# Kernel tuning notes

Hardware: AMD Instinct MI355X
Metric: run time of the kernel (lower is better)

Reference implementation:

```python
import jax, jax.numpy as jnp
import numpy as np

N_USER = 1_000_000
N_ITEM = 100_000
E = 16          # embedding_size
O = 16          # out_size per head
H = 4           # head_num
HID = 32        # hidden_size
B = 8192        # batch
S = 200         # sample_num
L = 50          # history length
NSUPP = 50_000  # supp_user_num


def _xavier(key, shape):
    fan_in, fan_out = shape[-2], shape[-1]
    std = np.sqrt(2.0 / (fan_in + fan_out))
    return (jax.random.normal(key, shape) * std).astype(jnp.float32)


def setup_inputs() -> dict:
    key = jax.random.key(0)
    ks = jax.random.split(key, 16)
    uid = jax.random.randint(ks[0], (B,), 0, N_USER)
    iid = jax.random.randint(ks[1], (B,), 0, N_ITEM)
    return {
        "user_embedding": _xavier(ks[2], (N_USER, E)),
        "item_embedding": _xavier(ks[3], (N_ITEM, E)),
        "wq": _xavier(ks[4], (H, E, O)),   # per-head Wq (no bias)
        "wk": _xavier(ks[5], (H, E, O)),
        "wv": _xavier(ks[6], (H, O, O)),
        "w_out": _xavier(ks[7], (H * O, O)),
        "l1_w": _xavier(ks[8], (3 * E, HID)),
        "l1_b": jnp.full((HID,), 0.1, jnp.float32),
        "l2_w": _xavier(ks[9], (HID, HID // 2)),
        "l2_b": jnp.full((HID // 2,), 0.1, jnp.float32),
        "l3_w": _xavier(ks[10], (HID // 2, 1)),
        "l3_b": jnp.full((1,), 0.1, jnp.float32),
        "user_bias": jnp.zeros((N_USER, 1), jnp.float32),
        "item_bias": jnp.zeros((N_ITEM, 1), jnp.float32),
        "x": jnp.stack([uid, iid], axis=1),                          # [B,2]
        "history": jax.random.randint(ks[11], (B, L), 0, N_ITEM),    # [B,L]
        "history_len": jax.random.randint(ks[12], (B,), 1, L + 1),   # [B] >=1
        "supp_users": jax.random.randint(ks[13], (NSUPP,), 0, N_USER),
        "sample_index": jax.random.randint(ks[14], (H, B, S), 0, NSUPP),
    }


def reference(user_embedding, item_embedding, wq, wk, wv, w_out,
              l1_w, l1_b, l2_w, l2_b, l3_w, l3_b, user_bias, item_bias,
              x, history, history_len, supp_users, sample_index):
    user_id = x[:, 0]
    item_id = x[:, 1]

    # user init embedding = mean-by-len of full (unmasked) history, as in source
    hist_emb = item_embedding[history]                                # [B,L,E]
    user_init = hist_emb.sum(axis=1) / history_len[:, None].astype(jnp.float32)  # [B,E]

    # per-head GAT over sampled support users (all heads vectorized)
    nb = user_embedding[supp_users[sample_index]]                     # [H,B,S,E]
    q = jnp.einsum('be,heo->hbo', user_init, wq)                      # [H,B,O]
    k = jnp.einsum('hbse,heo->hbso', nb, wk)                          # [H,B,S,O]
    attn = jax.nn.softmax(jnp.einsum('hbo,hbso->hbs', q, k), axis=-1)
    ctx = jnp.einsum('hbs,hbso->hbo', attn, k)                        # [H,B,O]
    gat = jnp.einsum('hbo,hop->hbp', ctx, wv)                         # [H,B,O]
    gat = jnp.transpose(gat, (1, 0, 2)).reshape(B, H * O)             # concat heads

    user_emb = gat @ w_out                                            # [B,O]
    item_emb = item_embedding[item_id]                                # [B,E]
    interaction = user_emb * item_emb
    ratings = interaction.sum(axis=1)

    h = jnp.concatenate([user_emb, item_emb, interaction], axis=1)    # [B,3E]
    x1 = jnp.tanh(h @ l1_w + l1_b)
    x2 = jnp.tanh(x1 @ l2_w + l2_b)
    x3 = (x2 @ l3_w + l3_b).reshape(-1)

    ub = user_bias[user_id, 0]
    ib = item_bias[item_id, 0]
    return (ratings + x3) / 2.0 + ub + ib
```

## Files before the change

kernel.cpp:

```cpp
#include <hip/hip_runtime.h>
#include <math.h>

#define N_USERS 1000000
#define N_ITEMS 100000
#define EMB 16
#define OUTD 16
#define NH 4
#define HID 32
#define BB 8192
#define SS 200
#define LL 50
#define NSUPP 50000

typedef float v4f __attribute__((ext_vector_type(4)));
typedef _Float16 h4 __attribute__((ext_vector_type(4)));
typedef _Float16 h2 __attribute__((ext_vector_type(2)));

__global__ __launch_bounds__(256) void prep_kernel(
    const float* __restrict__ user_emb,
    const int*   __restrict__ supp_users,
    const float* __restrict__ wk,
    _Float16*    __restrict__ Ksupp,
    const float* __restrict__ item_emb,
    const int*   __restrict__ history,
    const int*   __restrict__ history_len,
    const float* __restrict__ wq,
    float*       __restrict__ qbuf)
{
    __shared__ float s_wk[NH * EMB * OUTD];
    __shared__ float s_u[16][EMB];
    __shared__ float s_ui[4][EMB];
    __shared__ float s_wq[NH * EMB * OUTD];

    int t = threadIdx.x;
    if (blockIdx.x < NSUPP / 16) {
        for (int i = t; i < NH * EMB * OUTD; i += 256) s_wk[i] = wk[i];
        int n0 = blockIdx.x * 16;
        {
            int ul = t >> 4, e = t & 15;
            int row = supp_users[n0 + ul];
            s_u[ul][e] = user_emb[(size_t)row * EMB + e];
        }
        __syncthreads();
        int h   = t >> 6;
        int sub = (t >> 4) & 3;
        int o   = t & 15;
#pragma unroll
        for (int r = 0; r < 4; ++r) {
            int ul = sub + 4 * r;
            float acc = 0.f;
#pragma unroll
            for (int e = 0; e < EMB; ++e)
                acc += s_u[ul][e] * s_wk[(h * EMB + e) * OUTD + o];
            Ksupp[((size_t)h * NSUPP + n0 + ul) * OUTD + o] = (_Float16)acc;
        }
    } else {
        for (int i = t; i < NH * EMB * OUTD; i += 256) s_wq[i] = wq[i];
        int g    = t >> 6;
        int lane = t & 63;
        int l4   = lane >> 4;
        int e    = lane & 15;
        int b    = (blockIdx.x - NSUPP / 16) * 4 + g;

        float sum = 0.f;
        for (int l = l4; l < LL; l += 4) {
            int it = __builtin_nontemporal_load(history + (size_t)b * LL + l);
            sum += item_emb[(size_t)it * EMB + e];
        }
        sum += __shfl_xor(sum, 16);
        sum += __shfl_xor(sum, 32);
        if (lane < EMB) s_ui[g][lane] = sum / (float)history_len[b];
        __syncthreads();

        int h = (t >> 4) & 3;
        int o = t & 15;
        float acc = 0.f;
#pragma unroll
        for (int ee = 0; ee < EMB; ++ee)
            acc += s_ui[g][ee] * s_wq[(h * EMB + ee) * OUTD + o];
        qbuf[((size_t)b * NH + h) * OUTD + o] = acc;
    }
}

__global__ __launch_bounds__(256, 8) void attn_kernel(
    const _Float16* __restrict__ Ksupp,
    const float* __restrict__ qbuf,
    const int*   __restrict__ sample_index,
    const float* __restrict__ wv,
    float*       __restrict__ gat)
{
    int blk   = blockIdx.x;
    int h     = (blk & 7) >> 1;
    int btile = ((blk >> 3) << 1) | (blk & 1);
    int wave  = threadIdx.x >> 6;
    int lane  = threadIdx.x & 63;
    int b     = btile * 4 + wave;
    int g     = lane >> 2;
    int qt    = lane & 3;

    const int* si = sample_index + ((size_t)h * BB + b) * SS;
    int pre0 = __builtin_nontemporal_load(si + lane);
    int pre1 = __builtin_nontemporal_load(si + lane + 64);
    int pre2 = __builtin_nontemporal_load(si + lane + 128);
    int pre3 = (lane < 8) ? __builtin_nontemporal_load(si + lane + 192) : 0;

    v4f qv = __builtin_nontemporal_load(
        (const v4f*)(qbuf + ((size_t)b * NH + h) * OUTD) + qt);
    h4 qh = __builtin_convertvector(qv, h4);
    h2 qlo = {qh.x, qh.y};
    h2 qhi = {qh.z, qh.w};

    const h4* K4 = (const h4*)(Ksupp + (size_t)h * NSUPP * OUTD);

    int idx[13];
#pragma unroll
    for (int r = 0; r < 13; ++r) {
        int pre = (r < 4) ? pre0 : (r < 8) ? pre1 : (r < 12) ? pre2 : pre3;
        idx[r] = __shfl(pre, (r & 3) * 16 + g, 64);
    }

    h4 kq[13];
#pragma unroll
    for (int r = 0; r < 13; ++r)
        kq[r] = K4[idx[r] * 4 + qt];

    float l = 0.f;
    v4f c = {0.f, 0.f, 0.f, 0.f};
#pragma unroll
    for (int r = 0; r < 13; ++r) {
        h2 klo = {kq[r].x, kq[r].y};
        h2 khi = {kq[r].z, kq[r].w};
        float p = __builtin_amdgcn_fdot2(klo, qlo,
                  __builtin_amdgcn_fdot2(khi, qhi, 0.f, false), false);
        p += __shfl_xor(p, 1);
        p += __shfl_xor(p, 2);
        float w = __expf(p);
        if (r == 12) w = (g < 8) ? w : 0.f;
        l += w;
        v4f kf = __builtin_convertvector(kq[r], v4f);
        c += w * kf;
    }
#pragma unroll
    for (int off = 4; off < 64; off <<= 1) {
        l   += __shfl_xor(l, off);
        c.x += __shfl_xor(c.x, off);
        c.y += __shfl_xor(c.y, off);
        c.z += __shfl_xor(c.z, off);
        c.w += __shfl_xor(c.w, off);
    }
    float inv = 1.f / l;

    float part = c.x * wv[((size_t)h * OUTD + qt * 4 + 0) * OUTD + g]
               + c.y * wv[((size_t)h * OUTD + qt * 4 + 1) * OUTD + g]
               + c.z * wv[((size_t)h * OUTD + qt * 4 + 2) * OUTD + g]
               + c.w * wv[((size_t)h * OUTD + qt * 4 + 3) * OUTD + g];
    part += __shfl_xor(part, 1);
    part += __shfl_xor(part, 2);
    if (qt == 0)
        gat[(size_t)b * (NH * OUTD) + h * OUTD + g] = part * inv;
}

__global__ __launch_bounds__(256) void epilogue_kernel(
    const float* __restrict__ gat,
    const float* __restrict__ item_emb,
    const float* __restrict__ w_out,
    const float* __restrict__ l1_w, const float* __restrict__ l1_b,
    const float* __restrict__ l2_w, const float* __restrict__ l2_b,
    const float* __restrict__ l3_w, const float* __restrict__ l3_b,
    const float* __restrict__ user_bias, const float* __restrict__ item_bias,
    const int*   __restrict__ x,
    float*       __restrict__ out)
{
    int t    = threadIdx.x;
    int g    = t >> 6;
    int lane = t & 63;
    int b    = blockIdx.x * 4 + g;

    __shared__ float s_gat[4][NH * OUTD];
    __shared__ float s_ue[4][OUTD];
    __shared__ float s_ie[4][EMB];
    __shared__ float s_x1[4][HID];
    __shared__ float s_x2[4][HID / 2];

    int uid = x[(size_t)b * 2 + 0];
    int iid = x[(size_t)b * 2 + 1];

    s_gat[g][lane] = gat[(size_t)b * (NH * OUTD) + lane];
    if (lane < EMB) s_ie[g][lane] = item_emb[(size_t)iid * EMB + lane];
    __syncthreads();

    if (lane < OUTD) {
        float acc = 0.f;
#pragma unroll
        for (int j = 0; j < NH * OUTD; ++j) acc += s_gat[g][j] * w_out[j * OUTD + lane];
        s_ue[g][lane] = acc;
    }
    __syncthreads();

    if (lane < HID) {
        float acc = l1_b[lane];
#pragma unroll
        for (int i = 0; i < EMB; ++i) {
            float ue = s_ue[g][i], ie = s_ie[g][i];
            acc += ue * l1_w[i * HID + lane]
                 + ie * l1_w[(EMB + i) * HID + lane]
                 + ue * ie * l1_w[(2 * EMB + i) * HID + lane];
        }
        s_x1[g][lane] = tanhf(acc);
    }
    __syncthreads();

    if (lane < HID / 2) {
        float acc = l2_b[lane];
#pragma unroll
        for (int j = 0; j < HID; ++j) acc += s_x1[g][j] * l2_w[j * (HID / 2) + lane];
        s_x2[g][lane] = tanhf(acc);
    }
    __syncthreads();

    if (lane == 0) {
        float x3 = l3_b[0];
#pragma unroll
        for (int j = 0; j < HID / 2; ++j) x3 += s_x2[g][j] * l3_w[j];
        float ratings = 0.f;
#pragma unroll
        for (int o = 0; o < OUTD; ++o) ratings += s_ue[g][o] * s_ie[g][o];
        out[b] = 0.5f * (ratings + x3) + user_bias[uid] + item_bias[iid];
    }
}

extern "C" void kernel_launch(void* const* d_in, const int* in_sizes, int n_in,
                              void* d_out, int out_size, void* d_ws, size_t ws_size,
                              hipStream_t stream) {
    const float* user_embedding = (const float*)d_in[0];
    const float* item_embedding = (const float*)d_in[1];
    const float* wq             = (const float*)d_in[2];
    const float* wk             = (const float*)d_in[3];
    const float* wv             = (const float*)d_in[4];
    const float* w_out          = (const float*)d_in[5];
    const float* l1_w           = (const float*)d_in[6];
    const float* l1_b           = (const float*)d_in[7];
    const float* l2_w           = (const float*)d_in[8];
    const float* l2_b           = (const float*)d_in[9];
    const float* l3_w           = (const float*)d_in[10];
    const float* l3_b           = (const float*)d_in[11];
    const float* user_bias      = (const float*)d_in[12];
    const float* item_bias      = (const float*)d_in[13];
    const int*   x              = (const int*)d_in[14];
    const int*   history        = (const int*)d_in[15];
    const int*   history_len    = (const int*)d_in[16];
    const int*   supp_users     = (const int*)d_in[17];
    const int*   sample_index   = (const int*)d_in[18];
    float* out = (float*)d_out;

    char* ws = (char*)d_ws;
    _Float16* Ksupp = (_Float16*)ws;
    ws += (size_t)NH * NSUPP * OUTD * sizeof(_Float16);
    float* qbuf  = (float*)ws;
    ws += (size_t)BB * NH * OUTD * sizeof(float);
    float* gat   = (float*)ws;

    prep_kernel<<<NSUPP / 16 + BB / 4, 256, 0, stream>>>(
        user_embedding, supp_users, wk, Ksupp,
        item_embedding, history, history_len, wq, qbuf);
    attn_kernel<<<NH * BB / 4, 256, 0, stream>>>(Ksupp, qbuf, sample_index, wv, gat);
    epilogue_kernel<<<BB / 4, 256, 0, stream>>>(
        gat, item_embedding, w_out, l1_w, l1_b, l2_w, l2_b, l3_w, l3_b,
        user_bias, item_bias, x, out);
}
```

Measured before the change: 220.1 us.

## Use 16-byte K row loads with two lanes per sample in attention

The attention kernel now assigns two lanes per sampled neighbour, each loading 8 fp16 values (16 bytes), instead of four lanes each loading 4 values. This halves the gather instructions and the intra-group dot-product shuffles, and the last partial round is skipped for inactive lanes. In exchange the final reduction over 8 accumulators needs more cross-lane shuffles, register use rises, and the occupancy hint in launch bounds is lowered from 8 to 4.

```diff
diff --git a/kernel.cpp b/kernel.cpp
--- a/kernel.cpp
+++ b/kernel.cpp
@@ -13,8 +13,10 @@
 #define NSUPP 50000
 
 typedef float v4f __attribute__((ext_vector_type(4)));
+typedef float v8f __attribute__((ext_vector_type(8)));
+typedef _Float16 h2 __attribute__((ext_vector_type(2)));
 typedef _Float16 h4 __attribute__((ext_vector_type(4)));
-typedef _Float16 h2 __attribute__((ext_vector_type(2)));
+typedef _Float16 h8 __attribute__((ext_vector_type(8)));
 
 __global__ __launch_bounds__(256) void prep_kernel(
     const float* __restrict__ user_emb,
@@ -82,7 +84,7 @@
     }
 }
 
-__global__ __launch_bounds__(256, 8) void attn_kernel(
+__global__ __launch_bounds__(256, 4) void attn_kernel(
     const _Float16* __restrict__ Ksupp,
     const float* __restrict__ qbuf,
     const int*   __restrict__ sample_index,
@@ -95,8 +97,8 @@
     int wave  = threadIdx.x >> 6;
     int lane  = threadIdx.x & 63;
     int b     = btile * 4 + wave;
-    int g     = lane >> 2;
-    int qt    = lane & 3;
+    int g2    = lane >> 1;
+    int pr    = lane & 1;
 
     const int* si = sample_index + ((size_t)h * BB + b) * SS;
     int pre0 = __builtin_nontemporal_load(si + lane);
@@ -104,60 +106,68 @@
     int pre2 = __builtin_nontemporal_load(si + lane + 128);
     int pre3 = (lane < 8) ? __builtin_nontemporal_load(si + lane + 192) : 0;
 
-    v4f qv = __builtin_nontemporal_load(
-        (const v4f*)(qbuf + ((size_t)b * NH + h) * OUTD) + qt);
-    h4 qh = __builtin_convertvector(qv, h4);
-    h2 qlo = {qh.x, qh.y};
-    h2 qhi = {qh.z, qh.w};
-
-    const h4* K4 = (const h4*)(Ksupp + (size_t)h * NSUPP * OUTD);
-
-    int idx[13];
-#pragma unroll
-    for (int r = 0; r < 13; ++r) {
-        int pre = (r < 4) ? pre0 : (r < 8) ? pre1 : (r < 12) ? pre2 : pre3;
-        idx[r] = __shfl(pre, (r & 3) * 16 + g, 64);
-    }
-
-    h4 kq[13];
-#pragma unroll
-    for (int r = 0; r < 13; ++r)
-        kq[r] = K4[idx[r] * 4 + qt];
+    const v4f* qrow = (const v4f*)(qbuf + ((size_t)b * NH + h) * OUTD);
+    v4f qa = __builtin_nontemporal_load(qrow + pr * 2);
+    v4f qb = __builtin_nontemporal_load(qrow + pr * 2 + 1);
+    h4 qha = __builtin_convertvector(qa, h4);
+    h4 qhb = __builtin_convertvector(qb, h4);
+    h2 q0 = {qha.x, qha.y}, q1 = {qha.z, qha.w};
+    h2 q2 = {qhb.x, qhb.y}, q3 = {qhb.z, qhb.w};
+
+    const h8* K8 = (const h8*)(Ksupp + (size_t)h * NSUPP * OUTD);
+
+    int idx[7];
+#pragma unroll
+    for (int r = 0; r < 7; ++r) {
+        int pre = (r < 2) ? pre0 : (r < 4) ? pre1 : (r < 6) ? pre2 : pre3;
+        idx[r] = __shfl(pre, (r & 1) * 32 + g2, 64);
+    }
+
+    h8 kq[7];
+#pragma unroll
+    for (int r = 0; r < 6; ++r)
+        kq[r] = K8[(size_t)idx[r] * 2 + pr];
+    {
+        h8 kz = {};
+        if (g2 < 8) kz = K8[(size_t)idx[6] * 2 + pr];
+        kq[6] = kz;
+    }
 
     float l = 0.f;
-    v4f c = {0.f, 0.f, 0.f, 0.f};
-#pragma unroll
-    for (int r = 0; r < 13; ++r) {
-        h2 klo = {kq[r].x, kq[r].y};
-        h2 khi = {kq[r].z, kq[r].w};
-        float p = __builtin_amdgcn_fdot2(klo, qlo,
-                  __builtin_amdgcn_fdot2(khi, qhi, 0.f, false), false);
+    v8f c = {0.f, 0.f, 0.f, 0.f, 0.f, 0.f, 0.f, 0.f};
+#pragma unroll
+    for (int r = 0; r < 7; ++r) {
+        h2 k0 = __builtin_shufflevector(kq[r], kq[r], 0, 1);
+        h2 k1 = __builtin_shufflevector(kq[r], kq[r], 2, 3);
+        h2 k2 = __builtin_shufflevector(kq[r], kq[r], 4, 5);
+        h2 k3 = __builtin_shufflevector(kq[r], kq[r], 6, 7);
+        float p = __builtin_amdgcn_fdot2(k0, q0,
+                  __builtin_amdgcn_fdot2(k1, q1,
+                  __builtin_amdgcn_fdot2(k2, q2,
+                  __builtin_amdgcn_fdot2(k3, q3, 0.f, false), false), false), false);
         p += __shfl_xor(p, 1);
-        p += __shfl_xor(p, 2);
         float w = __expf(p);
-        if (r == 12) w = (g < 8) ? w : 0.f;
+        if (r == 6) w = (g2 < 8) ? w : 0.f;
         l += w;
-        v4f kf = __builtin_convertvector(kq[r], v4f);
-        c += w * kf;
-    }
-#pragma unroll
-    for (int off = 4; off < 64; off <<= 1) {
-        l   += __shfl_xor(l, off);
-        c.x += __shfl_xor(c.x, off);
-        c.y += __shfl_xor(c.y, off);
-        c.z += __shfl_xor(c.z, off);
-        c.w += __shfl_xor(c.w, off);
+        c += w * __builtin_convertvector(kq[r], v8f);
+    }
+
+#pragma unroll
+    for (int off = 2; off < 64; off <<= 1) {
+        l += __shfl_xor(l, off);
+#pragma unroll
+        for (int j = 0; j < 8; ++j) c[j] += __shfl_xor(c[j], off);
     }
     float inv = 1.f / l;
 
-    float part = c.x * wv[((size_t)h * OUTD + qt * 4 + 0) * OUTD + g]
-               + c.y * wv[((size_t)h * OUTD + qt * 4 + 1) * OUTD + g]
-               + c.z * wv[((size_t)h * OUTD + qt * 4 + 2) * OUTD + g]
-               + c.w * wv[((size_t)h * OUTD + qt * 4 + 3) * OUTD + g];
+    int pcol = g2 & 15;
+    const float* wvh = wv + ((size_t)h * OUTD + pr * 8) * OUTD + pcol;
+    float part = 0.f;
+#pragma unroll
+    for (int j = 0; j < 8; ++j) part += c[j] * wvh[(size_t)j * OUTD];
     part += __shfl_xor(part, 1);
-    part += __shfl_xor(part, 2);
-    if (qt == 0)
-        gat[(size_t)b * (NH * OUTD) + h * OUTD + g] = part * inv;
+    if (pr == 0 && g2 < 16)
+        gat[(size_t)b * (NH * OUTD) + h * OUTD + pcol] = part * inv;
 }
 
 __global__ __launch_bounds__(256) void epilogue_kernel(
```

Result: no change. 219.2 us (-0.4%).

## Stream support-key tiles through LDS and walk sorted sample indices per block

Applied to the files above, without the earlier changes.

The attention kernel now gives each block 128 batch rows of one head. Each wave bitonic-sorts its rows' 200 sample indices and stores them in shared memory. The block then streams the whole per-head K table through double-buffered LDS tiles of 1024 rows, and each row consumes its sorted indices that fall inside the current tile. This swaps random global gathers for sequential streaming plus LDS lookups, which is meant to cut scattered memory traffic. The cost is that every block reads all 50k keys per head, pays for the in-register sort, and runs a divergent ballot-driven inner loop, with larger LDS use and low occupancy.

```diff
diff --git a/kernel.cpp b/kernel.cpp
--- a/kernel.cpp
+++ b/kernel.cpp
@@ -12,9 +12,15 @@
 #define LL 50
 #define NSUPP 50000
 
+#define TT 1024
+#define NT ((NSUPP + TT - 1) / TT)
+#define GB 128
+
 typedef float v4f __attribute__((ext_vector_type(4)));
+typedef float v8f __attribute__((ext_vector_type(8)));
+typedef _Float16 h2 __attribute__((ext_vector_type(2)));
 typedef _Float16 h4 __attribute__((ext_vector_type(4)));
-typedef _Float16 h2 __attribute__((ext_vector_type(2)));
+typedef _Float16 h8 __attribute__((ext_vector_type(8)));
 
 __global__ __launch_bounds__(256) void prep_kernel(
     const float* __restrict__ user_emb,
@@ -82,82 +88,178 @@
     }
 }
 
-__global__ __launch_bounds__(256, 8) void attn_kernel(
+__global__ __launch_bounds__(512, 2) void attn_kernel(
     const _Float16* __restrict__ Ksupp,
     const float* __restrict__ qbuf,
     const int*   __restrict__ sample_index,
     const float* __restrict__ wv,
     float*       __restrict__ gat)
 {
+    __shared__ __align__(16) _Float16 s_tile[2][TT * OUTD];
+    __shared__ unsigned short s_idx[GB * 256];
+
     int blk   = blockIdx.x;
     int h     = (blk & 7) >> 1;
     int btile = ((blk >> 3) << 1) | (blk & 1);
     int wave  = threadIdx.x >> 6;
     int lane  = threadIdx.x & 63;
-    int b     = btile * 4 + wave;
+    int tid   = threadIdx.x;
     int g     = lane >> 2;
     int qt    = lane & 3;
 
-    const int* si = sample_index + ((size_t)h * BB + b) * SS;
-    int pre0 = __builtin_nontemporal_load(si + lane);
-    int pre1 = __builtin_nontemporal_load(si + lane + 64);
-    int pre2 = __builtin_nontemporal_load(si + lane + 128);
-    int pre3 = (lane < 8) ? __builtin_nontemporal_load(si + lane + 192) : 0;
-
-    v4f qv = __builtin_nontemporal_load(
-        (const v4f*)(qbuf + ((size_t)b * NH + h) * OUTD) + qt);
-    h4 qh = __builtin_convertvector(qv, h4);
-    h2 qlo = {qh.x, qh.y};
-    h2 qhi = {qh.z, qh.w};
-
-    const h4* K4 = (const h4*)(Ksupp + (size_t)h * NSUPP * OUTD);
-
-    int idx[13];
-#pragma unroll
-    for (int r = 0; r < 13; ++r) {
-        int pre = (r < 4) ? pre0 : (r < 8) ? pre1 : (r < 12) ? pre2 : pre3;
-        idx[r] = __shfl(pre, (r & 3) * 16 + g, 64);
-    }
-
-    h4 kq[13];
-#pragma unroll
-    for (int r = 0; r < 13; ++r)
-        kq[r] = K4[idx[r] * 4 + qt];
+    const char* Khb = (const char*)(Ksupp + (size_t)h * NSUPP * OUTD);
+    int b_base = btile * GB;
+
+    v4f st[4];
+#pragma unroll
+    for (int m = 0; m < 4; ++m)
+        st[m] = *(const v4f*)(Khb + (size_t)(m * 512 + tid) * 16);
+
+    {
+        const int* si0 = sample_index + ((size_t)h * BB + (b_base + wave * 16)) * SS;
+        unsigned n0 = (unsigned)__builtin_nontemporal_load(si0 + lane);
+        unsigned n1 = (unsigned)__builtin_nontemporal_load(si0 + 64 + lane);
+        unsigned n2 = (unsigned)__builtin_nontemporal_load(si0 + 128 + lane);
+        unsigned n3 = (lane < SS - 192) ?
+            (unsigned)__builtin_nontemporal_load(si0 + 192 + lane) : 0xFFFFu;
+        for (int bs = 0; bs < 16; ++bs) {
+            unsigned v[4] = {n0, n1, n2, n3};
+            if (bs < 15) {
+                const int* si = si0 + (size_t)(bs + 1) * SS;
+                n0 = (unsigned)__builtin_nontemporal_load(si + lane);
+                n1 = (unsigned)__builtin_nontemporal_load(si + 64 + lane);
+                n2 = (unsigned)__builtin_nontemporal_load(si + 128 + lane);
+                n3 = (lane < SS - 192) ?
+                    (unsigned)__builtin_nontemporal_load(si + 192 + lane) : 0xFFFFu;
+            }
+#pragma unroll
+            for (int kk = 2; kk <= 256; kk <<= 1) {
+#pragma unroll
+                for (int j = kk >> 1; j > 0; j >>= 1) {
+                    if (j >= 64) {
+                        const int jr = j >> 6;
+#pragma unroll
+                        for (int r = 0; r < 4; ++r) {
+                            if ((r & jr) == 0) {
+                                const int rp = r | jr;
+                                bool up = (((unsigned)(r * 64) & (unsigned)kk) == 0u);
+                                unsigned a = v[r], bq = v[rp];
+                                unsigned mn = a < bq ? a : bq;
+                                unsigned mx = a < bq ? bq : a;
+                                v[r]  = up ? mn : mx;
+                                v[rp] = up ? mx : mn;
+                            }
+                        }
+                    } else {
+#pragma unroll
+                        for (int r = 0; r < 4; ++r) {
+                            unsigned a = v[r];
+                            unsigned p = (unsigned)__shfl_xor((int)a, j, 64);
+                            int e = r * 64 + lane;
+                            bool lower = ((e & j) == 0);
+                            bool up    = ((e & kk) == 0);
+                            unsigned mn = a < p ? a : p;
+                            unsigned mx = a < p ? p : a;
+                            v[r] = (up == lower) ? mn : mx;
+                        }
+                    }
+                }
+            }
+            int bl = wave * 16 + bs;
+            s_idx[bl * 256 +       lane] = (unsigned short)v[0];
+            s_idx[bl * 256 +  64 + lane] = (unsigned short)v[1];
+            s_idx[bl * 256 + 128 + lane] = (unsigned short)v[2];
+            s_idx[bl * 256 + 192 + lane] = (unsigned short)v[3];
+        }
+    }
+
+    int b_local = wave * 16 + g;
+    int bfull   = b_base + b_local;
+    const v4f* qrow = (const v4f*)(qbuf + ((size_t)bfull * NH + h) * OUTD);
+    h4 A = __builtin_convertvector(qrow[0], h4);
+    h4 Bv = __builtin_convertvector(qrow[1], h4);
+    h4 Cv = __builtin_convertvector(qrow[2], h4);
+    h4 Dv = __builtin_convertvector(qrow[3], h4);
+    h2 q0 = {A.x, A.y},  q1 = {A.z, A.w};
+    h2 q2 = {Bv.x, Bv.y}, q3 = {Bv.z, Bv.w};
+    h2 q4 = {Cv.x, Cv.y}, q5 = {Cv.z, Cv.w};
+    h2 q6 = {Dv.x, Dv.y}, q7 = {Dv.z, Dv.w};
+
+#pragma unroll
+    for (int m = 0; m < 4; ++m)
+        *(v4f*)((char*)&s_tile[0][0] + (size_t)(m * 512 + tid) * 16) = st[m];
+    __syncthreads();
 
     float l = 0.f;
-    v4f c = {0.f, 0.f, 0.f, 0.f};
-#pragma unroll
-    for (int r = 0; r < 13; ++r) {
-        h2 klo = {kq[r].x, kq[r].y};
-        h2 khi = {kq[r].z, kq[r].w};
-        float p = __builtin_amdgcn_fdot2(klo, qlo,
-                  __builtin_amdgcn_fdot2(khi, qhi, 0.f, false), false);
-        p += __shfl_xor(p, 1);
-        p += __shfl_xor(p, 2);
-        float w = __expf(p);
-        if (r == 12) w = (g < 8) ? w : 0.f;
-        l += w;
-        v4f kf = __builtin_convertvector(kq[r], v4f);
-        c += w * kf;
-    }
-#pragma unroll
-    for (int off = 4; off < 64; off <<= 1) {
-        l   += __shfl_xor(l, off);
-        c.x += __shfl_xor(c.x, off);
-        c.y += __shfl_xor(c.y, off);
-        c.z += __shfl_xor(c.z, off);
-        c.w += __shfl_xor(c.w, off);
+    v8f cA = {0.f,0.f,0.f,0.f,0.f,0.f,0.f,0.f};
+    v8f cB = {0.f,0.f,0.f,0.f,0.f,0.f,0.f,0.f};
+    int ptr = 0;
+    const unsigned short* qlist = &s_idx[b_local * 256];
+
+    for (int t = 0; t < NT; ++t) {
+        int cur = t & 1;
+        if (t + 1 < NT) {
+#pragma unroll
+            for (int m = 0; m < 4; ++m)
+                st[m] = *(const v4f*)(Khb + (size_t)(t + 1) * (TT * OUTD * 2)
+                                          + (size_t)(m * 512 + tid) * 16);
+        }
+        int lo = t * TT;
+        int hi = lo + TT; if (hi > NSUPP) hi = NSUPP;
+        const h8* tile8 = (const h8*)&s_tile[cur][0];
+
+        bool qdone = false;
+        for (;;) {
+            int e = (int)qlist[ptr + qt];
+            bool valid = (!qdone) && (e < hi);
+            int row = valid ? (e - lo) : 0;
+            h8 k0 = tile8[row * 2];
+            h8 k1 = tile8[row * 2 + 1];
+            float p;
+            p = __builtin_amdgcn_fdot2(__builtin_shufflevector(k0, k0, 0, 1), q0, 0.f, false);
+            p = __builtin_amdgcn_fdot2(__builtin_shufflevector(k0, k0, 2, 3), q1, p, false);
+            p = __builtin_amdgcn_fdot2(__builtin_shufflevector(k0, k0, 4, 5), q2, p, false);
+            p = __builtin_amdgcn_fdot2(__builtin_shufflevector(k0, k0, 6, 7), q3, p, false);
+            p = __builtin_amdgcn_fdot2(__builtin_shufflevector(k1, k1, 0, 1), q4, p, false);
+            p = __builtin_amdgcn_fdot2(__builtin_shufflevector(k1, k1, 2, 3), q5, p, false);
+            p = __builtin_amdgcn_fdot2(__builtin_shufflevector(k1, k1, 4, 5), q6, p, false);
+            p = __builtin_amdgcn_fdot2(__builtin_shufflevector(k1, k1, 6, 7), q7, p, false);
+            float w = valid ? __expf(p) : 0.f;
+            l += w;
+            cA += w * __builtin_convertvector(k0, v8f);
+            cB += w * __builtin_convertvector(k1, v8f);
+            unsigned long long bal = __ballot(valid);
+            int hits = __popcll((bal >> (g * 4)) & 0xFull);
+            ptr += hits;
+            if (hits < 4) qdone = true;
+            if (__ballot(!qdone) == 0ull) break;
+        }
+
+        if (t + 1 < NT) {
+#pragma unroll
+            for (int m = 0; m < 4; ++m)
+                *(v4f*)((char*)&s_tile[cur ^ 1][0] + (size_t)(m * 512 + tid) * 16) = st[m];
+        }
+        __syncthreads();
+    }
+
+    l += __shfl_xor(l, 1); l += __shfl_xor(l, 2);
+#pragma unroll
+    for (int i = 0; i < 8; ++i) {
+        cA[i] += __shfl_xor(cA[i], 1); cA[i] += __shfl_xor(cA[i], 2);
+        cB[i] += __shfl_xor(cB[i], 1); cB[i] += __shfl_xor(cB[i], 2);
     }
     float inv = 1.f / l;
 
-    float part = c.x * wv[((size_t)h * OUTD + qt * 4 + 0) * OUTD + g]
-               + c.y * wv[((size_t)h * OUTD + qt * 4 + 1) * OUTD + g]
-               + c.z * wv[((size_t)h * OUTD + qt * 4 + 2) * OUTD + g]
-               + c.w * wv[((size_t)h * OUTD + qt * 4 + 3) * OUTD + g];
-    part += __shfl_xor(part, 1);
-    part += __shfl_xor(part, 2);
-    if (qt == 0)
-        gat[(size_t)b * (NH * OUTD) + h * OUTD + g] = part * inv;
+    v4f acc = {0.f, 0.f, 0.f, 0.f};
+    const float* wvh = wv + (size_t)h * OUTD * OUTD + qt * 4;
+#pragma unroll
+    for (int j = 0; j < 8; ++j) {
+        acc += cA[j] * *(const v4f*)(wvh + (size_t)j * OUTD);
+        acc += cB[j] * *(const v4f*)(wvh + (size_t)(j + 8) * OUTD);
+    }
+    acc *= inv;
+    *(v4f*)(gat + (size_t)bfull * (NH * OUTD) + h * OUTD + qt * 4) = acc;
 }
 
 __global__ __launch_bounds__(256) void epilogue_kernel(
@@ -263,7 +365,7 @@
     prep_kernel<<<NSUPP / 16 + BB / 4, 256, 0, stream>>>(
         user_embedding, supp_users, wk, Ksupp,
         item_embedding, history, history_len, wq, qbuf);
-    attn_kernel<<<NH * BB / 4, 256, 0, stream>>>(Ksupp, qbuf, sample_index, wv, gat);
+    attn_kernel<<<NH * BB / GB, 512, 0, stream>>>(Ksupp, qbuf, sample_index, wv, gat);
     epilogue_kernel<<<BB / 4, 256, 0, stream>>>(
         gat, item_embedding, w_out, l1_w, l1_b, l2_w, l2_b, l3_w, l3_b,
         user_bias, item_bias, x, out);
```

After: 281.0 us. 27.7% more time.

## Bucket samples by table slice and stream fp16 support table through LDS

Applied to the files above, without the earlier changes.

Attention is restructured so it no longer gathers per-head projected keys from global memory. Wk is folded into the query (q·Wkᵀ), and Wk·Wv is folded into a precomputed matrix. This lets the kernel work directly on a single fp16 gathered user-embedding table shared across heads. Each 512-thread block handles 32 batch rows across all 4 heads. It counting-sorts each row's 200 sample indices into 33 slices, then streams the table slice by slice through double-buffered LDS and does the dot products and accumulations from LDS. This replaces random global gathers with coalesced streaming. The cost is that every block reads the whole table, plus extra sort and atomic overhead and lower occupancy.

```diff
diff --git a/kernel.cpp b/kernel.cpp
--- a/kernel.cpp
+++ b/kernel.cpp
@@ -12,50 +12,49 @@
 #define LL 50
 #define NSUPP 50000
 
+#define SLICE_ROWS 1536
+#define NP 33
+#define TBL_ROWS (NP * SLICE_ROWS)
+#define SLICE_BYTES (SLICE_ROWS * EMB * 2)
+#define GBB 32
+
 typedef float v4f __attribute__((ext_vector_type(4)));
-typedef _Float16 h4 __attribute__((ext_vector_type(4)));
 typedef _Float16 h2 __attribute__((ext_vector_type(2)));
+typedef _Float16 h8 __attribute__((ext_vector_type(8)));
+
+#define WAVE_SYNC() do { asm volatile("s_waitcnt lgkmcnt(0)" ::: "memory"); \
+                         __builtin_amdgcn_sched_barrier(0); } while (0)
 
 __global__ __launch_bounds__(256) void prep_kernel(
     const float* __restrict__ user_emb,
     const int*   __restrict__ supp_users,
     const float* __restrict__ wk,
-    _Float16*    __restrict__ Ksupp,
+    const float* __restrict__ wq,
+    const float* __restrict__ wv,
     const float* __restrict__ item_emb,
     const int*   __restrict__ history,
     const int*   __restrict__ history_len,
-    const float* __restrict__ wq,
-    float*       __restrict__ qbuf)
+    _Float16*    __restrict__ tbl,
+    _Float16*    __restrict__ qtbuf,
+    float*       __restrict__ Wkv)
 {
-    __shared__ float s_wk[NH * EMB * OUTD];
-    __shared__ float s_u[16][EMB];
     __shared__ float s_ui[4][EMB];
     __shared__ float s_wq[NH * EMB * OUTD];
+    __shared__ float s_wk[NH * EMB * OUTD];
+    __shared__ float s_q[4][NH * OUTD];
 
     int t = threadIdx.x;
     if (blockIdx.x < NSUPP / 16) {
-        for (int i = t; i < NH * EMB * OUTD; i += 256) s_wk[i] = wk[i];
         int n0 = blockIdx.x * 16;
-        {
-            int ul = t >> 4, e = t & 15;
-            int row = supp_users[n0 + ul];
-            s_u[ul][e] = user_emb[(size_t)row * EMB + e];
-        }
-        __syncthreads();
-        int h   = t >> 6;
-        int sub = (t >> 4) & 3;
-        int o   = t & 15;
-#pragma unroll
-        for (int r = 0; r < 4; ++r) {
-            int ul = sub + 4 * r;
-            float acc = 0.f;
-#pragma unroll
-            for (int e = 0; e < EMB; ++e)
-                acc += s_u[ul][e] * s_wk[(h * EMB + e) * OUTD + o];
-            Ksupp[((size_t)h * NSUPP + n0 + ul) * OUTD + o] = (_Float16)acc;
-        }
-    } else {
-        for (int i = t; i < NH * EMB * OUTD; i += 256) s_wq[i] = wq[i];
+        int ul = t >> 4, e = t & 15;
+        int row = supp_users[n0 + ul];
+        tbl[(size_t)(n0 + ul) * EMB + e] =
+            (_Float16)user_emb[(size_t)row * EMB + e];
+    } else if (blockIdx.x < NSUPP / 16 + BB / 4) {
+        for (int i = t; i < NH * EMB * OUTD; i += 256) {
+            s_wq[i] = wq[i];
+            s_wk[i] = wk[i];
+        }
         int g    = t >> 6;
         int lane = t & 63;
         int l4   = lane >> 4;
@@ -78,86 +77,189 @@
 #pragma unroll
         for (int ee = 0; ee < EMB; ++ee)
             acc += s_ui[g][ee] * s_wq[(h * EMB + ee) * OUTD + o];
-        qbuf[((size_t)b * NH + h) * OUTD + o] = acc;
+        s_q[g][h * OUTD + o] = acc;
+        __syncthreads();
+
+        float qt = 0.f;
+#pragma unroll
+        for (int oo = 0; oo < OUTD; ++oo)
+            qt += s_wk[(h * EMB + o) * OUTD + oo] * s_q[g][h * OUTD + oo];
+        qtbuf[((size_t)b * NH + h) * EMB + o] = (_Float16)qt;
+    } else {
+        for (int i = t; i < NH * EMB * OUTD; i += 256) {
+            int h = i >> 8, e = (i >> 4) & 15, p = i & 15;
+            float a = 0.f;
+#pragma unroll
+            for (int o = 0; o < OUTD; ++o)
+                a += wk[(h * EMB + e) * OUTD + o] * wv[(h * OUTD + o) * OUTD + p];
+            Wkv[i] = a;
+        }
     }
 }
 
-__global__ __launch_bounds__(256, 8) void attn_kernel(
-    const _Float16* __restrict__ Ksupp,
-    const float* __restrict__ qbuf,
+__global__ __launch_bounds__(512, 2) void attn_kernel(
+    const _Float16* __restrict__ tbl,
+    const _Float16* __restrict__ qtbuf,
     const int*   __restrict__ sample_index,
-    const float* __restrict__ wv,
+    const float* __restrict__ Wkv,
     float*       __restrict__ gat)
 {
-    int blk   = blockIdx.x;
-    int h     = (blk & 7) >> 1;
-    int btile = ((blk >> 3) << 1) | (blk & 1);
-    int wave  = threadIdx.x >> 6;
-    int lane  = threadIdx.x & 63;
-    int b     = btile * 4 + wave;
-    int g     = lane >> 2;
-    int qt    = lane & 3;
-
-    const int* si = sample_index + ((size_t)h * BB + b) * SS;
-    int pre0 = __builtin_nontemporal_load(si + lane);
-    int pre1 = __builtin_nontemporal_load(si + lane + 64);
-    int pre2 = __builtin_nontemporal_load(si + lane + 128);
-    int pre3 = (lane < 8) ? __builtin_nontemporal_load(si + lane + 192) : 0;
-
-    v4f qv = __builtin_nontemporal_load(
-        (const v4f*)(qbuf + ((size_t)b * NH + h) * OUTD) + qt);
-    h4 qh = __builtin_convertvector(qv, h4);
-    h2 qlo = {qh.x, qh.y};
-    h2 qhi = {qh.z, qh.w};
-
-    const h4* K4 = (const h4*)(Ksupp + (size_t)h * NSUPP * OUTD);
-
-    int idx[13];
-#pragma unroll
-    for (int r = 0; r < 13; ++r) {
-        int pre = (r < 4) ? pre0 : (r < 8) ? pre1 : (r < 12) ? pre2 : pre3;
-        idx[r] = __shfl(pre, (r & 3) * 16 + g, 64);
-    }
-
-    h4 kq[13];
-#pragma unroll
-    for (int r = 0; r < 13; ++r)
-        kq[r] = K4[idx[r] * 4 + qt];
+    __shared__ __align__(16) _Float16 s_slice[2][SLICE_ROWS * EMB];
+    __shared__ unsigned short s_list[128 * SS];
+    __shared__ unsigned char  s_cnt[128][36];
+    __shared__ unsigned int   s_hist[8][40];
+
+    int tid  = threadIdx.x;
+    int wave = tid >> 6;
+    int lane = tid & 63;
+    int g    = lane >> 2;
+    int qt   = lane & 3;
+    int hb   = wave * 16 + g;
+    int h    = hb & 3;
+    int bl   = hb >> 2;
+    int bfull = blockIdx.x * GBB + bl;
+
+    v4f stg[6];
+#pragma unroll
+    for (int i = 0; i < 6; ++i)
+        stg[i] = *(const v4f*)((const char*)tbl + (size_t)i * 8192 + (size_t)tid * 16);
+
+    for (int bs = 0; bs < 16; ++bs) {
+        int hbs = wave * 16 + bs;
+        int hs = hbs & 3, bls = hbs >> 2;
+        const int* si = sample_index + ((size_t)hs * BB + (blockIdx.x * GBB + bls)) * SS;
+        int v0 = __builtin_nontemporal_load(si + lane);
+        int v1 = __builtin_nontemporal_load(si + lane + 64);
+        int v2 = __builtin_nontemporal_load(si + lane + 128);
+        int v3 = (lane < SS - 192) ? __builtin_nontemporal_load(si + lane + 192) : -1;
+
+        if (lane < NP + 1) s_hist[wave][lane] = 0;
+        WAVE_SYNC();
+        int b0 = ((v0 >> 9) * 21846) >> 16;
+        int b1 = ((v1 >> 9) * 21846) >> 16;
+        int b2 = ((v2 >> 9) * 21846) >> 16;
+        int b3 = (v3 >= 0) ? (((v3 >> 9) * 21846) >> 16) : 0;
+        atomicAdd(&s_hist[wave][b0], 1u);
+        atomicAdd(&s_hist[wave][b1], 1u);
+        atomicAdd(&s_hist[wave][b2], 1u);
+        if (v3 >= 0) atomicAdd(&s_hist[wave][b3], 1u);
+        WAVE_SYNC();
+        if (lane == 0) {
+            unsigned run = 0;
+            for (int k = 0; k < NP; ++k) {
+                unsigned c = s_hist[wave][k];
+                s_cnt[hbs][k] = (unsigned char)c;
+                s_hist[wave][k] = run;
+                run += c;
+            }
+        }
+        WAVE_SYNC();
+        unsigned p0 = atomicAdd(&s_hist[wave][b0], 1u);
+        s_list[hbs * SS + p0] = (unsigned short)v0;
+        unsigned p1 = atomicAdd(&s_hist[wave][b1], 1u);
+        s_list[hbs * SS + p1] = (unsigned short)v1;
+        unsigned p2 = atomicAdd(&s_hist[wave][b2], 1u);
+        s_list[hbs * SS + p2] = (unsigned short)v2;
+        if (v3 >= 0) {
+            unsigned p3 = atomicAdd(&s_hist[wave][b3], 1u);
+            s_list[hbs * SS + p3] = (unsigned short)v3;
+        }
+        WAVE_SYNC();
+    }
+
+    const h8* qtp = (const h8*)(qtbuf + ((size_t)bfull * NH + h) * EMB);
+    h8 qA = qtp[0], qB = qtp[1];
+    h2 tq0 = __builtin_shufflevector(qA, qA, 0, 1);
+    h2 tq1 = __builtin_shufflevector(qA, qA, 2, 3);
+    h2 tq2 = __builtin_shufflevector(qA, qA, 4, 5);
+    h2 tq3 = __builtin_shufflevector(qA, qA, 6, 7);
+    h2 tq4 = __builtin_shufflevector(qB, qB, 0, 1);
+    h2 tq5 = __builtin_shufflevector(qB, qB, 2, 3);
+    h2 tq6 = __builtin_shufflevector(qB, qB, 4, 5);
+    h2 tq7 = __builtin_shufflevector(qB, qB, 6, 7);
+
+#pragma unroll
+    for (int i = 0; i < 6; ++i)
+        *(v4f*)((char*)&s_slice[0][0] + (size_t)i * 8192 + (size_t)tid * 16) = stg[i];
+    __syncthreads();
 
     float l = 0.f;
-    v4f c = {0.f, 0.f, 0.f, 0.f};
-#pragma unroll
-    for (int r = 0; r < 13; ++r) {
-        h2 klo = {kq[r].x, kq[r].y};
-        h2 khi = {kq[r].z, kq[r].w};
-        float p = __builtin_amdgcn_fdot2(klo, qlo,
-                  __builtin_amdgcn_fdot2(khi, qhi, 0.f, false), false);
-        p += __shfl_xor(p, 1);
-        p += __shfl_xor(p, 2);
-        float w = __expf(p);
-        if (r == 12) w = (g < 8) ? w : 0.f;
-        l += w;
-        v4f kf = __builtin_convertvector(kq[r], v4f);
-        c += w * kf;
-    }
-#pragma unroll
-    for (int off = 4; off < 64; off <<= 1) {
-        l   += __shfl_xor(l, off);
-        c.x += __shfl_xor(c.x, off);
-        c.y += __shfl_xor(c.y, off);
-        c.z += __shfl_xor(c.z, off);
-        c.w += __shfl_xor(c.w, off);
+    float cu[16];
+#pragma unroll
+    for (int j = 0; j < 16; ++j) cu[j] = 0.f;
+    int base = 0;
+
+    for (int p = 0; p < NP; ++p) {
+        if (p + 1 < NP) {
+            size_t sb = (size_t)(p + 1) * SLICE_BYTES;
+#pragma unroll
+            for (int i = 0; i < 6; ++i)
+                stg[i] = *(const v4f*)((const char*)tbl + sb + (size_t)i * 8192
+                                        + (size_t)tid * 16);
+        }
+        const h8* sl = (const h8*)&s_slice[p & 1][0];
+        int cnt = (int)s_cnt[hb][p];
+        int pbase = p * SLICE_ROWS;
+
+        for (int it = 0;; ++it) {
+            int off = it * 4 + qt;
+            bool valid = off < cnt;
+            if (__ballot(valid) == 0ull) break;
+            int pos = valid ? base + off : 0;
+            int v   = (int)s_list[hb * SS + pos];
+            int rl  = valid ? v - pbase : 0;
+            h8 u0 = sl[rl * 2];
+            h8 u1 = sl[rl * 2 + 1];
+            h2 a0 = __builtin_shufflevector(u0, u0, 0, 1);
+            h2 a1 = __builtin_shufflevector(u0, u0, 2, 3);
+            h2 a2 = __builtin_shufflevector(u0, u0, 4, 5);
+            h2 a3 = __builtin_shufflevector(u0, u0, 6, 7);
+            h2 a4 = __builtin_shufflevector(u1, u1, 0, 1);
+            h2 a5 = __builtin_shufflevector(u1, u1, 2, 3);
+            h2 a6 = __builtin_shufflevector(u1, u1, 4, 5);
+            h2 a7 = __builtin_shufflevector(u1, u1, 6, 7);
+            float s = __builtin_amdgcn_fdot2(a0, tq0,
+                      __builtin_amdgcn_fdot2(a1, tq1,
+                      __builtin_amdgcn_fdot2(a2, tq2,
+                      __builtin_amdgcn_fdot2(a3, tq3,
+                      __builtin_amdgcn_fdot2(a4, tq4,
+                      __builtin_amdgcn_fdot2(a5, tq5,
+                      __builtin_amdgcn_fdot2(a6, tq6,
+                      __builtin_amdgcn_fdot2(a7, tq7,
+                      0.f, false), false), false), false),
+                      false), false), false), false);
+            float w = valid ? __expf(s) : 0.f;
+            l += w;
+#pragma unroll
+            for (int j = 0; j < 8; ++j) cu[j]     += w * (float)u0[j];
+#pragma unroll
+            for (int j = 0; j < 8; ++j) cu[8 + j] += w * (float)u1[j];
+        }
+        base += cnt;
+        __syncthreads();
+        if (p + 1 < NP) {
+#pragma unroll
+            for (int i = 0; i < 6; ++i)
+                *(v4f*)((char*)&s_slice[(p + 1) & 1][0] + (size_t)i * 8192
+                        + (size_t)tid * 16) = stg[i];
+        }
+        __syncthreads();
+    }
+
+    l += __shfl_xor(l, 1);
+    l += __shfl_xor(l, 2);
+#pragma unroll
+    for (int j = 0; j < 16; ++j) {
+        cu[j] += __shfl_xor(cu[j], 1);
+        cu[j] += __shfl_xor(cu[j], 2);
     }
     float inv = 1.f / l;
-
-    float part = c.x * wv[((size_t)h * OUTD + qt * 4 + 0) * OUTD + g]
-               + c.y * wv[((size_t)h * OUTD + qt * 4 + 1) * OUTD + g]
-               + c.z * wv[((size_t)h * OUTD + qt * 4 + 2) * OUTD + g]
-               + c.w * wv[((size_t)h * OUTD + qt * 4 + 3) * OUTD + g];
-    part += __shfl_xor(part, 1);
-    part += __shfl_xor(part, 2);
-    if (qt == 0)
-        gat[(size_t)b * (NH * OUTD) + h * OUTD + g] = part * inv;
+    v4f acc = {0.f, 0.f, 0.f, 0.f};
+#pragma unroll
+    for (int e = 0; e < EMB; ++e)
+        acc += cu[e] * *(const v4f*)(Wkv + ((size_t)(h * EMB + e) * OUTD) + qt * 4);
+    acc *= inv;
+    *(v4f*)(gat + (size_t)bfull * (NH * OUTD) + h * OUTD + qt * 4) = acc;
 }
 
 __global__ __launch_bounds__(256) void epilogue_kernel(
@@ -254,16 +356,18 @@
     float* out = (float*)d_out;
 
     char* ws = (char*)d_ws;
-    _Float16* Ksupp = (_Float16*)ws;
-    ws += (size_t)NH * NSUPP * OUTD * sizeof(_Float16);
-    float* qbuf  = (float*)ws;
+    _Float16* tbl = (_Float16*)ws;
+    ws += (size_t)TBL_ROWS * EMB * sizeof(_Float16);
+    _Float16* qtbuf = (_Float16*)ws;
+    ws += (size_t)BB * NH * EMB * sizeof(_Float16);
+    float* gat = (float*)ws;
     ws += (size_t)BB * NH * OUTD * sizeof(float);
-    float* gat   = (float*)ws;
-
-    prep_kernel<<<NSUPP / 16 + BB / 4, 256, 0, stream>>>(
-        user_embedding, supp_users, wk, Ksupp,
-        item_embedding, history, history_len, wq, qbuf);
-    attn_kernel<<<NH * BB / 4, 256, 0, stream>>>(Ksupp, qbuf, sample_index, wv, gat);
+    float* Wkv = (float*)ws;
+
+    prep_kernel<<<NSUPP / 16 + BB / 4 + 1, 256, 0, stream>>>(
+        user_embedding, supp_users, wk, wq, wv,
+        item_embedding, history, history_len, tbl, qtbuf, Wkv);
+    attn_kernel<<<BB / GBB, 512, 0, stream>>>(tbl, qtbuf, sample_index, Wkv, gat);
     epilogue_kernel<<<BB / 4, 256, 0, stream>>>(
         gat, item_embedding, w_out, l1_w, l1_b, l2_w, l2_b, l3_w, l3_b,
         user_bias, item_bias, x, out);
```

Result: slower. 243.0 us (+10.4%).
